# Kernel optimization log

Measured on AMD Instinct MI355X. Metric: run time of the kernel, lower is better.

## Reference

```python
import jax, jax.numpy as jnp
import numpy as np

N = 8192
DIMS = 128
HID = 64
NEG = -9e15


def setup_inputs() -> dict:
    key = jax.random.key(0)
    k_adj, k_h, k_w1, k_w2 = jax.random.split(key, 4)
    graph_info = (jax.random.uniform(k_adj, (N, N)) < 0.01).astype(jnp.float32)
    h = jax.random.normal(k_h, (N, DIMS), dtype=jnp.float32)
    # xavier-normal-ish init for the 2-layer scoring MLP (dims -> 64 -> 1)
    W1 = jax.random.normal(k_w1, (DIMS, HID), dtype=jnp.float32) * np.sqrt(2.0 / (DIMS + HID))
    b1 = jnp.zeros((HID,), dtype=jnp.float32)
    W2 = jax.random.normal(k_w2, (HID, 1), dtype=jnp.float32) * np.sqrt(2.0 / (HID + 1))
    b2 = jnp.zeros((1,), dtype=jnp.float32)
    return {"graph_info": graph_info, "h": h, "W1": W1, "b1": b1, "W2": W2, "b2": b2}


def reference(graph_info, h, W1, b1, W2, b2):
    # per-node MLP score: e_j for every node j  -> [N, 1]
    e = jnp.dot(jnp.maximum(jnp.dot(h, W1) + b1, 0.0), W2) + b2
    # e.transpose().repeat(N,1): row i sees scores of all columns j -> broadcast [1, N]
    scores = e[:, 0][None, :]
    # mask non-edges with large negative, softmax over neighbors (dim=-1)
    att = jnp.where(graph_info > 0, scores, jnp.float32(NEG))
    att = jax.nn.softmax(att, axis=-1)
    out = jnp.dot(att, h)  # [N, dims] aggregation
    # sum_flag == 1: rescale each row by its degree (diagflat(num) @ h)
    num = jnp.sum(graph_info, axis=-1)  # [N]
    out = num[:, None] * out
    return out
```

## Files before the change

### kernel.cpp

```cpp
#include <hip/hip_runtime.h>
#include <math.h>

#define NN 8192
#define DIMS 128
#define HID 64
#define CAP 192

typedef float f4v __attribute__((ext_vector_type(4)));
typedef float f2v __attribute__((ext_vector_type(2)));
typedef unsigned short u16x8 __attribute__((ext_vector_type(8)));
typedef unsigned long long u64;

__global__ __launch_bounds__(256) void score_kernel(
    const float* __restrict__ h, const float* __restrict__ W1,
    const float* __restrict__ b1, const float* __restrict__ W2,
    const float* __restrict__ b2, float* __restrict__ ee) {
  __shared__ float sW1[DIMS * HID];
  for (int i = threadIdx.x * 4; i < DIMS * HID; i += 1024)
    *(float4*)&sW1[i] = *(const float4*)&W1[i];
  __syncthreads();
  int wv = threadIdx.x >> 6, lane = threadIdx.x & 63;
  int j0 = blockIdx.x * 16 + wv * 4;
  const f4v* h4 = (const f4v*)(h + (size_t)j0 * DIMS);
  float bb = b1[lane];
  float a0 = bb, a1 = bb, a2 = bb, a3 = bb;
#pragma unroll 8
  for (int d4 = 0; d4 < 32; ++d4) {
    f4v v0 = h4[d4], v1 = h4[d4 + 32], v2 = h4[d4 + 64], v3 = h4[d4 + 96];
    float w0 = sW1[(d4 * 4 + 0) * HID + lane];
    float w1 = sW1[(d4 * 4 + 1) * HID + lane];
    float w2c = sW1[(d4 * 4 + 2) * HID + lane];
    float w3 = sW1[(d4 * 4 + 3) * HID + lane];
    a0 = fmaf(v0.x, w0, a0); a0 = fmaf(v0.y, w1, a0); a0 = fmaf(v0.z, w2c, a0); a0 = fmaf(v0.w, w3, a0);
    a1 = fmaf(v1.x, w0, a1); a1 = fmaf(v1.y, w1, a1); a1 = fmaf(v1.z, w2c, a1); a1 = fmaf(v1.w, w3, a1);
    a2 = fmaf(v2.x, w0, a2); a2 = fmaf(v2.y, w1, a2); a2 = fmaf(v2.z, w2c, a2); a2 = fmaf(v2.w, w3, a2);
    a3 = fmaf(v3.x, w0, a3); a3 = fmaf(v3.y, w1, a3); a3 = fmaf(v3.z, w2c, a3); a3 = fmaf(v3.w, w3, a3);
  }
  float w2 = W2[lane];
  float r0 = fmaxf(a0, 0.f) * w2, r1 = fmaxf(a1, 0.f) * w2;
  float r2 = fmaxf(a2, 0.f) * w2, r3 = fmaxf(a3, 0.f) * w2;
#pragma unroll
  for (int off = 32; off > 0; off >>= 1) {
    r0 += __shfl_xor(r0, off, 64);
    r1 += __shfl_xor(r1, off, 64);
    r2 += __shfl_xor(r2, off, 64);
    r3 += __shfl_xor(r3, off, 64);
  }
  if (lane == 0) {
    float bo = b2[0];
    ee[j0]     = expf(r0 + bo);
    ee[j0 + 1] = expf(r1 + bo);
    ee[j0 + 2] = expf(r2 + bo);
    ee[j0 + 3] = expf(r3 + bo);
  }
}

#define NIBBLE(v)                                                              \
  ((u64)(((__float_as_uint((v).x) >> 29) & 1u) |                               \
         ((__float_as_uint((v).y) >> 28) & 2u) |                               \
         ((__float_as_uint((v).z) >> 27) & 4u) |                               \
         ((__float_as_uint((v).w) >> 26) & 8u)))

__device__ __forceinline__ void gather_batch8(
    const unsigned short* sidx, int q, int cnt,
    const float* __restrict__ ee, const float* __restrict__ hb,
    float& ax, float& ay, float& z) {
  if (q >= cnt) return;
  u16x8 jv = *(const u16x8*)(sidx + q);
  int j[8];
#pragma unroll
  for (int k = 0; k < 8; ++k) j[k] = (q + k < cnt) ? (int)jv[k] : 0;
  float wv[8];
#pragma unroll
  for (int k = 0; k < 8; ++k) wv[k] = ee[j[k]];
  f2v hv[8];
#pragma unroll
  for (int k = 0; k < 8; ++k) hv[k] = *(const f2v*)(hb + (size_t)j[k] * DIMS);
#pragma unroll
  for (int k = 0; k < 8; ++k) {
    float m = (q + k < cnt) ? wv[k] : 0.f;
    z += m;
    ax = fmaf(m, hv[k].x, ax);
    ay = fmaf(m, hv[k].y, ay);
  }
}

__global__ __launch_bounds__(256) void pc_kernel(
    const float* __restrict__ graph, const float* __restrict__ h,
    const float* __restrict__ ee, float* __restrict__ out) {
  __shared__ unsigned short s_idx[4][CAP];
  volatile __shared__ int s_flag[4];
  int w = threadIdx.x >> 6, lane = threadIdx.x & 63;
  int rbase = blockIdx.x * 4;
  if (threadIdx.x < 4) s_flag[threadIdx.x] = 0;
  __syncthreads();

  if (w < 2) {
    u64 lt = (1ull << lane) - 1ull;
#pragma unroll 1
    for (int i = 0; i < 2; ++i) {
      int s = w * 2 + i;
      int row = rbase + s;
      const f4v* g4 = (const f4v*)(graph + (size_t)row * NN) + lane;
      u64 a0 = 0, a1 = 0;
      f4v c0 = g4[0], c1 = g4[64], c2 = g4[128], c3 = g4[192];
#pragma unroll
      for (int t = 0; t < 8; ++t) {
        f4v n0, n1, n2, n3;
        if (t < 7) {
          const f4v* nb2 = g4 + (t * 4 + 4) * 64;
          n0 = nb2[0]; n1 = nb2[64]; n2 = nb2[128]; n3 = nb2[192];
        }
        {
          u64 q0 = NIBBLE(c0), q1 = NIBBLE(c1), q2 = NIBBLE(c2), q3 = NIBBLE(c3);
          int c = t * 4;
          if (c < 16)     a0 |= q0 << (4 * (c & 15));       else a1 |= q0 << (4 * (c & 15));
          if (c + 1 < 16) a0 |= q1 << (4 * ((c + 1) & 15)); else a1 |= q1 << (4 * ((c + 1) & 15));
          if (c + 2 < 16) a0 |= q2 << (4 * ((c + 2) & 15)); else a1 |= q2 << (4 * ((c + 2) & 15));
          if (c + 3 < 16) a0 |= q3 << (4 * ((c + 3) & 15)); else a1 |= q3 << (4 * ((c + 3) & 15));
        }
        if (t < 7) { c0 = n0; c1 = n1; c2 = n2; c3 = n3; }
      }
      int t0 = (int)__popcll(a0), t1 = (int)__popcll(a1);
      int tot = t0 + t1, incl = tot;
#pragma unroll
      for (int d = 1; d < 64; d <<= 1) {
        int vsh = __shfl_up(incl, d, 64);
        if (lane >= d) incl += vsh;
      }
      int base = incl - tot;
      int cnt = __shfl(incl, 63, 64);
      unsigned short* dst = &s_idx[s][0];
      int pidx = base;
      u64 m = a0;
      while (m) {
        int bit = __ffsll(m) - 1;
        int col = ((bit >> 2) << 8) + lane * 4 + (bit & 3);
        if (pidx < CAP) dst[pidx] = (unsigned short)col;
        ++pidx; m &= m - 1;
      }
      m = a1;
      while (m) {
        int bit = __ffsll(m) - 1;
        int col = 4096 + ((bit >> 2) << 8) + lane * 4 + (bit & 3);
        if (pidx < CAP) dst[pidx] = (unsigned short)col;
        ++pidx; m &= m - 1;
      }
      cnt = cnt < CAP ? cnt : CAP;
      __threadfence_block();
      if (lane == 0) s_flag[s] = cnt + 1;
    }
  } else {
    const float* hb = h + lane * 2;
#pragma unroll 1
    for (int i = 0; i < 2; ++i) {
      int s = (w - 2) * 2 + i;
      int row = rbase + s;
      int f;
      while ((f = s_flag[s]) == 0) __builtin_amdgcn_s_sleep(1);
      __threadfence_block();
      int cnt = f - 1;
      float ax = 0.f, ay = 0.f, z = 0.f;
#pragma unroll 1
      for (int q = 0; q < cnt; q += 8)
        gather_batch8(&s_idx[s][0], q, cnt, ee, hb, ax, ay, z);
      float scale = cnt > 0 ? (float)cnt / z : 0.f;
      f2v o2; o2.x = ax * scale; o2.y = ay * scale;
      *(f2v*)(out + (size_t)row * DIMS + lane * 2) = o2;
    }
  }
}

extern "C" void kernel_launch(void* const* d_in, const int* in_sizes, int n_in,
                              void* d_out, int out_size, void* d_ws, size_t ws_size,
                              hipStream_t stream) {
  const float* graph = (const float*)d_in[0];
  const float* h     = (const float*)d_in[1];
  const float* W1    = (const float*)d_in[2];
  const float* b1    = (const float*)d_in[3];
  const float* W2    = (const float*)d_in[4];
  const float* b2    = (const float*)d_in[5];
  float* out = (float*)d_out;
  float* ee  = (float*)d_ws;

  score_kernel<<<NN / 16, 256, 0, stream>>>(h, W1, b1, W2, b2, ee);
  pc_kernel<<<NN / 4, 256, 0, stream>>>(graph, h, ee, out);
}
```

Measured before the change: 79.02 us.

## Premultiply h by scores into bf16 table to halve gather bytes

```diff
diff --git a/kernel.cpp b/kernel.cpp
--- a/kernel.cpp
+++ b/kernel.cpp
@@ -55,6 +55,23 @@
   }
 }
 
+__device__ __forceinline__ unsigned int f2bf(float f) {
+  unsigned u = __float_as_uint(f);
+  return (u + 0x7fffu + ((u >> 16) & 1u)) >> 16;
+}
+
+__global__ __launch_bounds__(256) void gbuild_kernel(
+    const float* __restrict__ h, const float* __restrict__ ee,
+    unsigned int* __restrict__ g) {
+  int i = blockIdx.x * 256 + threadIdx.x;
+  int j = i >> 6;
+  float eej = ee[j];
+  f2v hv = *(const f2v*)(h + (size_t)i * 2);
+  unsigned lo = f2bf(hv.x * eej);
+  unsigned hi = f2bf(hv.y * eej);
+  g[i] = lo | (hi << 16);
+}
+
 #define NIBBLE(v)                                                              \
   ((u64)(((__float_as_uint((v).x) >> 29) & 1u) |                               \
          ((__float_as_uint((v).y) >> 28) & 2u) |                               \
@@ -63,30 +80,32 @@
 
 __device__ __forceinline__ void gather_batch8(
     const unsigned short* sidx, int q, int cnt,
-    const float* __restrict__ ee, const float* __restrict__ hb,
+    const float* __restrict__ ee, const unsigned int* __restrict__ gb,
     float& ax, float& ay, float& z) {
   if (q >= cnt) return;
   u16x8 jv = *(const u16x8*)(sidx + q);
   int j[8];
 #pragma unroll
-  for (int k = 0; k < 8; ++k) j[k] = (q + k < cnt) ? (int)jv[k] : 0;
+  for (int k = 0; k < 8; ++k) j[k] = (int)jv[k];
   float wv[8];
 #pragma unroll
   for (int k = 0; k < 8; ++k) wv[k] = ee[j[k]];
-  f2v hv[8];
-#pragma unroll
-  for (int k = 0; k < 8; ++k) hv[k] = *(const f2v*)(hb + (size_t)j[k] * DIMS);
+  unsigned hv[8];
+#pragma unroll
+  for (int k = 0; k < 8; ++k) hv[k] = gb[(size_t)j[k] * 64];
 #pragma unroll
   for (int k = 0; k < 8; ++k) {
-    float m = (q + k < cnt) ? wv[k] : 0.f;
-    z += m;
-    ax = fmaf(m, hv[k].x, ax);
-    ay = fmaf(m, hv[k].y, ay);
+    bool vld = (q + k < cnt);
+    z += vld ? wv[k] : 0.f;
+    float gx = __uint_as_float(hv[k] << 16);
+    float gy = __uint_as_float(hv[k] & 0xffff0000u);
+    ax += vld ? gx : 0.f;
+    ay += vld ? gy : 0.f;
   }
 }
 
 __global__ __launch_bounds__(256) void pc_kernel(
-    const float* __restrict__ graph, const float* __restrict__ h,
+    const float* __restrict__ graph, const unsigned int* __restrict__ g,
     const float* __restrict__ ee, float* __restrict__ out) {
   __shared__ unsigned short s_idx[4][CAP];
   volatile __shared__ int s_flag[4];
@@ -151,7 +170,7 @@
       if (lane == 0) s_flag[s] = cnt + 1;
     }
   } else {
-    const float* hb = h + lane * 2;
+    const unsigned int* gb = g + lane;
 #pragma unroll 1
     for (int i = 0; i < 2; ++i) {
       int s = (w - 2) * 2 + i;
@@ -163,7 +182,7 @@
       float ax = 0.f, ay = 0.f, z = 0.f;
 #pragma unroll 1
       for (int q = 0; q < cnt; q += 8)
-        gather_batch8(&s_idx[s][0], q, cnt, ee, hb, ax, ay, z);
+        gather_batch8(&s_idx[s][0], q, cnt, ee, gb, ax, ay, z);
       float scale = cnt > 0 ? (float)cnt / z : 0.f;
       f2v o2; o2.x = ax * scale; o2.y = ay * scale;
       *(f2v*)(out + (size_t)row * DIMS + lane * 2) = o2;
@@ -181,8 +200,11 @@
   const float* W2    = (const float*)d_in[4];
   const float* b2    = (const float*)d_in[5];
   float* out = (float*)d_out;
-  float* ee  = (float*)d_ws;
+
+  float* ee = (float*)d_ws;
+  unsigned int* g = (unsigned int*)((char*)d_ws + NN * sizeof(float));
 
   score_kernel<<<NN / 16, 256, 0, stream>>>(h, W1, b1, W2, b2, ee);
-  pc_kernel<<<NN / 4, 256, 0, stream>>>(graph, h, ee, out);
-}
+  gbuild_kernel<<<NN * DIMS / 2 / 256, 256, 0, stream>>>(h, ee, g);
+  pc_kernel<<<NN / 4, 256, 0, stream>>>(graph, g, ee, out);
+}
```

Measured after the change: 75.04 us. 5.0% less time.
